# Kernel optimization log

Hardware: AMD Instinct MI355X
Metric: run time of the kernel (lower is better)

## Reference

```python
import jax, jax.numpy as jnp
import numpy as np

B, S, H = 4, 1024, 1024
R = 512          # num_rules
M = 1024         # memory_size
HEADS = 16
STEPS = 3        # inference_steps
TEMP = 1.0       # softmax_temperature
LN_EPS = 1e-5


def setup_inputs() -> dict:
    key = jax.random.key(0)
    ks = jax.random.split(key, 40)
    std = 0.02
    p = lambda k, shp: (jax.random.normal(k, shp, jnp.float32) * std)
    inp = {
        "hidden_states": jax.random.normal(ks[0], (B, S, H), jnp.float32),
        "rule_embeddings": p(ks[1], (R, H)),
        "rule_sel_w": p(ks[2], (H, R)), "rule_sel_b": jnp.zeros((R,), jnp.float32),
        # self-attention (nn.MultiheadAttention) projections
        "attn_wq": p(ks[3], (H, H)), "attn_bq": jnp.zeros((H,), jnp.float32),
        "attn_wk": p(ks[4], (H, H)), "attn_bk": jnp.zeros((H,), jnp.float32),
        "attn_wv": p(ks[5], (H, H)), "attn_bv": jnp.zeros((H,), jnp.float32),
        "attn_wo": p(ks[6], (H, H)), "attn_bo": jnp.zeros((H,), jnp.float32),
        # memory bank + key/query/value projections
        "memory": p(ks[7], (M, H)),
        "mem_q_w": p(ks[8], (H, H)), "mem_q_b": jnp.zeros((H,), jnp.float32),
        "mem_k_w": p(ks[9], (H, H)), "mem_k_b": jnp.zeros((H,), jnp.float32),
        "mem_v_w": p(ks[10], (H, H)), "mem_v_b": jnp.zeros((H,), jnp.float32),
        # memory_attention (nn.MultiheadAttention) projections
        "mattn_wq": p(ks[11], (H, H)), "mattn_bq": jnp.zeros((H,), jnp.float32),
        "mattn_wk": p(ks[12], (H, H)), "mattn_bk": jnp.zeros((H,), jnp.float32),
        "mattn_wv": p(ks[13], (H, H)), "mattn_bv": jnp.zeros((H,), jnp.float32),
        "mattn_wo": p(ks[14], (H, H)), "mattn_bo": jnp.zeros((H,), jnp.float32),
        # rule_application: Linear(2H,H)+LN+GELU+Linear(H,H)
        "ra_w1": p(ks[15], (2 * H, H)), "ra_b1": jnp.zeros((H,), jnp.float32),
        "ra_ln_s": jnp.ones((H,), jnp.float32), "ra_ln_b": jnp.zeros((H,), jnp.float32),
        "ra_w2": p(ks[16], (H, H)), "ra_b2": jnp.zeros((H,), jnp.float32),
        # confidence_scorer
        "conf_w": p(ks[17], (H, 1)), "conf_b": jnp.zeros((1,), jnp.float32),
    }
    return inp


def _mha(q_in, k_in, v_in, wq, bq, wk, bk, wv, bv, wo, bo):
    # standard nn.MultiheadAttention math (batch_first, eval mode -> no dropout)
    b, sq, h = q_in.shape
    d = h // HEADS
    qh = (q_in @ wq + bq).reshape(b, sq, HEADS, d)
    kh = (k_in @ wk + bk).reshape(b, -1, HEADS, d)
    vh = (v_in @ wv + bv).reshape(b, -1, HEADS, d)
    scores = jnp.einsum('bqhd,bkhd->bhqk', qh, kh) / jnp.sqrt(jnp.asarray(d, qh.dtype))
    probs = jax.nn.softmax(scores, axis=-1)
    out = jnp.einsum('bhqk,bkhd->bqhd', probs, vh).reshape(b, sq, h)
    return out @ wo + bo


def _ln(x, s, b):
    mu = x.mean(-1, keepdims=True)
    var = ((x - mu) ** 2).mean(-1, keepdims=True)
    return (x - mu) / jnp.sqrt(var + LN_EPS) * s + b


def reference(hidden_states, rule_embeddings, rule_sel_w, rule_sel_b,
              attn_wq, attn_bq, attn_wk, attn_bk, attn_wv, attn_bv, attn_wo, attn_bo,
              memory, mem_q_w, mem_q_b, mem_k_w, mem_k_b, mem_v_w, mem_v_b,
              mattn_wq, mattn_bq, mattn_wk, mattn_bk, mattn_wv, mattn_bv, mattn_wo, mattn_bo,
              ra_w1, ra_b1, ra_ln_s, ra_ln_b, ra_w2, ra_b2, conf_w, conf_b):
    h = hidden_states
    b = h.shape[0]
    # memory keys/values are input-independent: project once, broadcast over batch
    mk = jnp.broadcast_to((memory @ mem_k_w + mem_k_b)[None], (b, M, H))
    mv = jnp.broadcast_to((memory @ mem_v_w + mem_v_b)[None], (b, M, H))
    for _ in range(STEPS):
        # rule routing: soft selection over the rule-embedding table
        rule_probs = jax.nn.softmax((h @ rule_sel_w + rule_sel_b) / TEMP, axis=-1)  # [B,S,R]
        selected = jnp.einsum('bsr,rh->bsh', rule_probs, rule_embeddings)           # [B,S,H]
        # self-attention reasoning
        h = h + _mha(h, h, h, attn_wq, attn_bq, attn_wk, attn_bk,
                     attn_wv, attn_bv, attn_wo, attn_bo)
        # memory attention
        mq = h @ mem_q_w + mem_q_b
        h = h + _mha(mq, mk, mv, mattn_wq, mattn_bq, mattn_wk, mattn_bk,
                     mattn_wv, mattn_bv, mattn_wo, mattn_bo)
        # rule application MLP on [h ; selected_rules]
        x = jnp.concatenate([h, selected], axis=-1)                                  # [B,S,2H]
        u = jax.nn.gelu(_ln(x @ ra_w1 + ra_b1, ra_ln_s, ra_ln_b), approximate=False)
        h = h + (u @ ra_w2 + ra_b2)
    confidence = jax.nn.sigmoid(h @ conf_w + conf_b)  # [B,S,1]
    return h, confidence
```

## Files before the change

kernel.cpp:

```cpp
#include <hip/hip_runtime.h>
#include <stdint.h>

typedef _Float16 f16;
typedef __attribute__((ext_vector_type(4))) float floatx4;
typedef __attribute__((ext_vector_type(8))) f16   f16x8;
typedef __attribute__((ext_vector_type(4))) f16   f16x4;

#define GLD_LDS16(gp, lp)                                                                      \
  __builtin_amdgcn_global_load_lds((const __attribute__((address_space(1))) void*)(uintptr_t)(gp), \
                                   (__attribute__((address_space(3))) void*)(uintptr_t)(lp), 16, 0, 0)

struct SrlOut {
  int n0;
  const float* bias;
  const float* resid;
  float* Cf; f16* Cb;
  int ldcf, ldcb, transV;
  long long sCb, sCh;
};
struct SrlGemmArgs {
  const f16* A; const f16* B;
  int M, N, K, lda, ldb;
  long long sAb, sAh, sBb, sBh;
  float alpha;
  int nOuts;
  SrlOut out[4];
};

template<int BM, int BN, int MINW>
__global__ __launch_bounds__(256, MINW) void srl_gemm(SrlGemmArgs g) {
  constexpr int BK = 64;
  constexpr int ACH = BM / 32;
  constexpr int BCH = BN / 32;
  constexpr int MI  = (BM == 128 && BN == 128) ? 4 : 2;
  constexpr int NI  = (BN == 128) ? 4 : ((BM == 128) ? 4 : 2);
  __shared__ f16 As[BM * BK];
  __shared__ f16 Bs[BN * BK];
  const int tid  = threadIdx.x;
  const int wid  = tid >> 6;
  const int lane = tid & 63;
  const int z  = blockIdx.z, zh = z & 15, zb = z >> 4;

  const int gx = gridDim.x;
  const int NT = gx * gridDim.y;
  const int L  = blockIdx.y * gx + blockIdx.x;
  const int W  = ((NT & 7) == 0) ? ((L & 7) * (NT >> 3) + (L >> 3)) : L;
  const int tn = (W % gx) * BN;
  const int tm = (W / gx) * BM;

  const f16* Ab = g.A + (long long)zb * g.sAb + (long long)zh * g.sAh + (long long)tm * g.lda;
  const f16* Bb = g.B + (long long)zb * g.sBb + (long long)zh * g.sBh + (long long)tn * g.ldb;
  const int maxAr = g.M - 1 - tm;
  const int maxBr = g.N - 1 - tn;

  int aR[ACH], aO[ACH];
#pragma unroll
  for (int i = 0; i < ACH; ++i) {
    int e = wid * (BM * 16) + i * 512 + lane * 8;
    int r = e >> 6, s = (e >> 3) & 7;
    aR[i] = r; aO[i] = ((s - r) & 7) * 8;
  }
  int bR[BCH], bO[BCH];
#pragma unroll
  for (int i = 0; i < BCH; ++i) {
    int e = wid * (BN * 16) + i * 512 + lane * 8;
    int r = e >> 6, s = (e >> 3) & 7;
    bR[i] = r; bO[i] = ((s - r) & 7) * 8;
  }
  f16* lA = As + wid * (BM * 16);
  f16* lB = Bs + wid * (BN * 16);

  floatx4 acc[MI][NI];
#pragma unroll
  for (int a = 0; a < MI; ++a)
#pragma unroll
    for (int b = 0; b < NI; ++b) {
      acc[a][b][0] = 0.f; acc[a][b][1] = 0.f; acc[a][b][2] = 0.f; acc[a][b][3] = 0.f;
    }

  const int wm = (BM == 128 && BN == 128) ? (wid & 1) * 64
               : (BN == 128)              ? 0
               : (BM == 128)              ? wid * 32
                                          : (wid & 1) * 32;
  const int wn = (BM == 128 && BN == 128) ? (wid >> 1) * 64
               : (BM == 64 && BN == 64)   ? (wid >> 1) * 32
                                          : 0;
  const int lm = lane & 15;
  const int quad = lane >> 4;

  for (int k0 = 0; k0 < g.K; k0 += BK) {
    __syncthreads();
#pragma unroll
    for (int i = 0; i < ACH; ++i) {
      int r = aR[i] <= maxAr ? aR[i] : maxAr;
      GLD_LDS16(Ab + (long long)r * g.lda + (k0 + aO[i]), lA + i * 512);
    }
#pragma unroll
    for (int i = 0; i < BCH; ++i) {
      int r = bR[i] <= maxBr ? bR[i] : maxBr;
      GLD_LDS16(Bb + (long long)r * g.ldb + (k0 + bO[i]), lB + i * 512);
    }
    __syncthreads();
#pragma unroll
    for (int ks = 0; ks < 2; ++ks) {
      f16x8 af[MI], bfr[NI];
#pragma unroll
      for (int mi = 0; mi < MI; ++mi) {
        int row = wm + mi * 16 + lm;
        int sg = ((ks * 4 + quad) + row) & 7;
        af[mi] = *(const f16x8*)(As + row * 64 + sg * 8);
      }
#pragma unroll
      for (int ni = 0; ni < NI; ++ni) {
        int row = wn + ni * 16 + lm;
        int sg = ((ks * 4 + quad) + row) & 7;
        bfr[ni] = *(const f16x8*)(Bs + row * 64 + sg * 8);
      }
#pragma unroll
      for (int mi = 0; mi < MI; ++mi)
#pragma unroll
        for (int ni = 0; ni < NI; ++ni)
          acc[mi][ni] = __builtin_amdgcn_mfma_f32_16x16x32_f16(af[mi], bfr[ni], acc[mi][ni], 0, 0, 0);
    }
  }

  int oi = 0;
  for (int j = 1; j < g.nOuts; ++j)
    if (tn >= g.out[j].n0) oi = j;
  const SrlOut O = g.out[oi];
  const long long zc = (long long)zb * O.sCb + (long long)zh * O.sCh;
#pragma unroll
  for (int mi = 0; mi < MI; ++mi) {
#pragma unroll
    for (int r = 0; r < 4; ++r) {
      int m = tm + wm + mi * 16 + quad * 4 + r;
      if (m >= g.M) continue;
#pragma unroll
      for (int ni = 0; ni < NI; ++ni) {
        int n = tn + wn + ni * 16 + lm;
        if (n >= g.N) continue;
        int nl = n - O.n0;
        float v = acc[mi][ni][r] * g.alpha;
        if (O.bias)  v += O.bias[nl];
        if (O.resid) v += O.resid[(long long)m * O.ldcf + nl];
        if (O.Cf)    O.Cf[zc + (long long)m * O.ldcf + nl] = v;
        if (O.Cb) {
          long long idx = O.transV
              ? ((long long)(m >> 10) * 1048576 + (long long)nl * 1024 + (m & 1023))
              : (zc + (long long)m * O.ldcb + nl);
          O.Cb[idx] = (f16)v;
        }
      }
    }
  }
}

__global__ __launch_bounds__(512, 4) void srl_gemm_p(SrlGemmArgs g) {
  __shared__ f16 As[2][8192];
  __shared__ f16 Bs[2][8192];
  const int tid  = threadIdx.x;
  const int wid  = tid >> 6;
  const int lane = tid & 63;

  const int gx  = gridDim.x;
  const int NTt = gx * gridDim.y;
  const int L   = blockIdx.y * gx + blockIdx.x;
  const int W   = ((NTt & 7) == 0) ? ((L & 7) * (NTt >> 3) + (L >> 3)) : L;
  const int tn  = (W % gx) * 128;
  const int tm  = (W / gx) * 128;

  const f16* Ab = g.A + (long long)tm * g.lda;
  const f16* Bb = g.B + (long long)tn * g.ldb;

  int aR[2], aO[2];
#pragma unroll
  for (int i = 0; i < 2; ++i) {
    int e = wid * 1024 + i * 512 + lane * 8;
    int r = e >> 6, s = (e >> 3) & 7;
    aR[i] = r; aO[i] = ((s - r) & 7) * 8;
  }

  const int wm = (wid >> 1) * 32;
  const int wn = (wid & 1) * 64;
  const int lm = lane & 15;
  const int quad = lane >> 4;

  floatx4 acc[2][4];
#pragma unroll
  for (int a = 0; a < 2; ++a)
#pragma unroll
    for (int b = 0; b < 4; ++b) {
      acc[a][b][0] = 0.f; acc[a][b][1] = 0.f; acc[a][b][2] = 0.f; acc[a][b][3] = 0.f;
    }

  const int nk = g.K >> 6;

  auto stage = [&](int kt, int bsel) {
    const int k0 = kt << 6;
    f16* lA = &As[bsel][0] + wid * 1024;
    f16* lB = &Bs[bsel][0] + wid * 1024;
#pragma unroll
    for (int i = 0; i < 2; ++i)
      GLD_LDS16(Ab + (long long)aR[i] * g.lda + (k0 + aO[i]), lA + i * 512);
#pragma unroll
    for (int i = 0; i < 2; ++i)
      GLD_LDS16(Bb + (long long)aR[i] * g.ldb + (k0 + aO[i]), lB + i * 512);
  };

  stage(0, 0);
  asm volatile("s_waitcnt vmcnt(0)" ::: "memory");
  __builtin_amdgcn_s_barrier();

  auto onestep = [&](int t, int cb) {
    if (t + 1 < nk) stage(t + 1, cb ^ 1);
    asm volatile("" ::: "memory");
    const f16* Asb = &As[cb][0];
    const f16* Bsb = &Bs[cb][0];
#pragma unroll
    for (int ks = 0; ks < 2; ++ks) {
      f16x8 af[2], bfr[4];
#pragma unroll
      for (int mi = 0; mi < 2; ++mi) {
        int row = wm + mi * 16 + lm;
        int sg = ((ks * 4 + quad) + row) & 7;
        af[mi] = *(const f16x8*)(Asb + row * 64 + sg * 8);
      }
#pragma unroll
      for (int ni = 0; ni < 4; ++ni) {
        int row = wn + ni * 16 + lm;
        int sg = ((ks * 4 + quad) + row) & 7;
        bfr[ni] = *(const f16x8*)(Bsb + row * 64 + sg * 8);
      }
#pragma unroll
      for (int mi = 0; mi < 2; ++mi)
#pragma unroll
        for (int ni = 0; ni < 4; ++ni)
          acc[mi][ni] = __builtin_amdgcn_mfma_f32_16x16x32_f16(af[mi], bfr[ni], acc[mi][ni], 0, 0, 0);
    }
    asm volatile("s_waitcnt vmcnt(0) lgkmcnt(0)" ::: "memory");
    __builtin_amdgcn_s_barrier();
  };

  for (int t = 0; t < nk; t += 2) {
    onestep(t, 0);
    onestep(t + 1, 1);
  }

  int oi = 0;
  for (int j = 1; j < g.nOuts; ++j)
    if (tn >= g.out[j].n0) oi = j;
  const SrlOut O = g.out[oi];
#pragma unroll
  for (int mi = 0; mi < 2; ++mi) {
#pragma unroll
    for (int r = 0; r < 4; ++r) {
      int m = tm + wm + mi * 16 + quad * 4 + r;
#pragma unroll
      for (int ni = 0; ni < 4; ++ni) {
        int n = tn + wn + ni * 16 + lm;
        int nl = n - O.n0;
        float v = acc[mi][ni][r] * g.alpha;
        if (O.bias)  v += O.bias[nl];
        if (O.resid) v += O.resid[(long long)m * O.ldcf + nl];
        if (O.Cf)    O.Cf[(long long)m * O.ldcf + nl] = v;
        if (O.Cb) {
          long long idx = O.transV
              ? ((long long)(m >> 10) * 1048576 + (long long)nl * 1024 + (m & 1023))
              : ((long long)m * O.ldcb + nl);
          O.Cb[idx] = (f16)v;
        }
      }
    }
  }
}

struct SrlFlashArgs {
  const f16* Q; const f16* K; const f16* VT; f16* O;
  long long sQb, sKb, sVb;
  float scale;
};

__global__ __launch_bounds__(256, 2) void srl_flash(SrlFlashArgs a) {
  __shared__ f16 Qs[8192];
  __shared__ f16 Ks[8192];
  __shared__ f16 VTs[8192];
  __shared__ f16 Ps[4][4096];
  const int tid = threadIdx.x, wid = tid >> 6, lane = tid & 63;
  const int quad = lane >> 4, c = lane & 15;
  const int L = blockIdx.x;
  const int bh = (L & 7) + ((L >> 6) << 3);
  const int qt = (L >> 3) & 7;
  const int b = bh >> 4, h = bh & 15;
  const f16* Qg = a.Q + (long long)b * a.sQb + (long long)qt * 131072 + h * 64;
  const f16* Kg = a.K + (long long)b * a.sKb + h * 64;
  const f16* Vg = a.VT + (long long)b * a.sVb + (long long)h * 65536;
  f16* Og = a.O + (long long)b * 1048576 + (long long)qt * 131072 + h * 64;

  int rRow[4], rOff[4];
#pragma unroll
  for (int i = 0; i < 4; ++i) {
    int e = wid * 2048 + i * 512 + lane * 8;
    int r = e >> 6, gL = (e >> 3) & 7;
    rRow[i] = r; rOff[i] = ((gL - r) & 7) * 8;
  }
  int vRow[4], vOff[4];
#pragma unroll
  for (int i = 0; i < 4; ++i) {
    int e = wid * 2048 + i * 512 + lane * 8;
    int d = e >> 7, gL = (e >> 3) & 15;
    vRow[i] = d; vOff[i] = ((gL - (d & 7)) & 15) * 8;
  }

#pragma unroll
  for (int i = 0; i < 4; ++i)
    GLD_LDS16(Qg + (long long)rRow[i] * 1024 + rOff[i], Qs + wid * 2048 + i * 512);
  __syncthreads();

  const int wq = wid * 32;
  f16x8 qf[2][2];
#pragma unroll
  for (int nf = 0; nf < 2; ++nf)
#pragma unroll
    for (int ch = 0; ch < 2; ++ch) {
      int row = wq + nf * 16 + c;
      int slot = ((ch * 4 + quad) + row) & 7;
      f16x8 v = *(const f16x8*)(Qs + row * 64 + slot * 8);
      f16 sc = (f16)a.scale;
#pragma unroll
      for (int j = 0; j < 8; ++j) v[j] = v[j] * sc;
      qf[nf][ch] = v;
    }

  float l_s[2] = {0.f, 0.f};
  floatx4 Oa[2][4];
#pragma unroll
  for (int nf = 0; nf < 2; ++nf)
#pragma unroll
    for (int no = 0; no < 4; ++no) {
      Oa[nf][no][0] = 0.f; Oa[nf][no][1] = 0.f; Oa[nf][no][2] = 0.f; Oa[nf][no][3] = 0.f;
    }

  for (int t = 0; t < 8; ++t) {
    __syncthreads();
#pragma unroll
    for (int i = 0; i < 4; ++i)
      GLD_LDS16(Kg + (long long)(t * 128 + rRow[i]) * 1024 + rOff[i], Ks + wid * 2048 + i * 512);
#pragma unroll
    for (int i = 0; i < 4; ++i)
      GLD_LDS16(Vg + (long long)vRow[i] * 1024 + (t * 128 + vOff[i]), VTs + wid * 2048 + i * 512);
    __syncthreads();

    floatx4 sT[2][8];
#pragma unroll
    for (int nf = 0; nf < 2; ++nf)
#pragma unroll
      for (int mf = 0; mf < 8; ++mf) {
        sT[nf][mf][0] = 0.f; sT[nf][mf][1] = 0.f; sT[nf][mf][2] = 0.f; sT[nf][mf][3] = 0.f;
      }
#pragma unroll
    for (int ch = 0; ch < 2; ++ch)
#pragma unroll
      for (int mf = 0; mf < 8; ++mf) {
        int key = mf * 16 + c;
        int slot = ((ch * 4 + quad) + key) & 7;
        f16x8 kf = *(const f16x8*)(Ks + key * 64 + slot * 8);
        sT[0][mf] = __builtin_amdgcn_mfma_f32_16x16x32_f16(kf, qf[0][ch], sT[0][mf], 0, 0, 0);
        sT[1][mf] = __builtin_amdgcn_mfma_f32_16x16x32_f16(kf, qf[1][ch], sT[1][mf], 0, 0, 0);
      }

#pragma unroll
    for (int nf = 0; nf < 2; ++nf) {
      float lt = 0.f;
      const int q = nf * 16 + c;
#pragma unroll
      for (int mf = 0; mf < 8; ++mf) {
        f16x4 pk;
#pragma unroll
        for (int r = 0; r < 4; ++r) {
          float p = __builtin_amdgcn_exp2f(sT[nf][mf][r]);
          lt += p;
          pk[r] = (f16)p;
        }
        int kg = mf * 2 + (quad >> 1), sub = (quad & 1) * 4;
        int slot = (kg + (q & 7)) & 15;
        *(f16x4*)(Ps[wid] + q * 128 + slot * 8 + sub) = pk;
      }
      lt += __shfl_xor(lt, 16);
      lt += __shfl_xor(lt, 32);
      l_s[nf] += lt;
    }
#pragma unroll
    for (int cc = 0; cc < 4; ++cc) {
      f16x8 af[2];
#pragma unroll
      for (int nf = 0; nf < 2; ++nf) {
        int q = nf * 16 + c;
        int slot = ((cc * 4 + quad) + (q & 7)) & 15;
        af[nf] = *(const f16x8*)(Ps[wid] + q * 128 + slot * 8);
      }
#pragma unroll
      for (int no = 0; no < 4; ++no) {
        int d = no * 16 + c;
        int slot = ((cc * 4 + quad) + (d & 7)) & 15;
        f16x8 vf = *(const f16x8*)(VTs + d * 128 + slot * 8);
        Oa[0][no] = __builtin_amdgcn_mfma_f32_16x16x32_f16(af[0], vf, Oa[0][no], 0, 0, 0);
        Oa[1][no] = __builtin_amdgcn_mfma_f32_16x16x32_f16(af[1], vf, Oa[1][no], 0, 0, 0);
      }
    }
  }

#pragma unroll
  for (int nf = 0; nf < 2; ++nf)
#pragma unroll
    for (int r = 0; r < 4; ++r) {
      float li = 1.f / __shfl(l_s[nf], quad * 4 + r);
      int qrow = wq + nf * 16 + quad * 4 + r;
#pragma unroll
      for (int no = 0; no < 4; ++no)
        Qs[qrow * 64 + no * 16 + c] = (f16)(Oa[nf][no][r] * li);
    }
  __syncthreads();
#pragma unroll
  for (int i = 0; i < 4; ++i) {
    int e = wid * 2048 + i * 512 + lane * 8;
    int row = e >> 6, col = e & 63;
    *(f16x8*)(Og + (long long)row * 1024 + col) = *(const f16x8*)(Qs + e);
  }
}

__global__ __launch_bounds__(256) void srl_softmax_rule(const float* logits, f16* probs) {
  __shared__ float red[16];
  const long long row = blockIdx.x;
  const float* p = logits + row * 512;
  const int tid = threadIdx.x;
  float v0 = p[tid], v1 = p[tid + 256];
  float mx = fmaxf(v0, v1);
#pragma unroll
  for (int o = 32; o > 0; o >>= 1) mx = fmaxf(mx, __shfl_down(mx, o));
  const int wid = tid >> 6, lane = tid & 63;
  if (lane == 0) red[wid] = mx;
  __syncthreads();
  if (tid == 0) red[8] = fmaxf(fmaxf(red[0], red[1]), fmaxf(red[2], red[3]));
  __syncthreads();
  mx = red[8];
  float e0 = __expf(v0 - mx), e1 = __expf(v1 - mx);
  float s = e0 + e1;
#pragma unroll
  for (int o = 32; o > 0; o >>= 1) s += __shfl_down(s, o);
  if (lane == 0) red[wid + 4] = s;
  __syncthreads();
  if (tid == 0) red[9] = 1.f / (red[4] + red[5] + red[6] + red[7]);
  __syncthreads();
  const float inv = red[9];
  probs[row * 512 + tid] = (f16)(e0 * inv);
  probs[row * 512 + tid + 256] = (f16)(e1 * inv);
}

__global__ __launch_bounds__(256) void srl_ln_gelu(const float* x, const float* gam, const float* bet, f16* out) {
  __shared__ float red[16];
  const long long row = blockIdx.x;
  const float* p = x + row * 1024;
  const int tid = threadIdx.x;
  float4 xv = *(const float4*)(p + tid * 4);
  float v[4] = {xv.x, xv.y, xv.z, xv.w};
  float s = v[0] + v[1] + v[2] + v[3];
  float s2 = v[0] * v[0] + v[1] * v[1] + v[2] * v[2] + v[3] * v[3];
#pragma unroll
  for (int o = 32; o > 0; o >>= 1) { s += __shfl_down(s, o); s2 += __shfl_down(s2, o); }
  const int wid = tid >> 6, lane = tid & 63;
  if (lane == 0) { red[wid] = s; red[wid + 4] = s2; }
  __syncthreads();
  if (tid == 0) {
    float ts = red[0] + red[1] + red[2] + red[3];
    float ts2 = red[4] + red[5] + red[6] + red[7];
    float mu = ts * (1.f / 1024.f);
    float var = ts2 * (1.f / 1024.f) - mu * mu;
    red[8] = mu;
    red[9] = rsqrtf(var + 1e-5f);
  }
  __syncthreads();
  const float mu = red[8], rstd = red[9];
  f16x4 o4;
#pragma unroll
  for (int i = 0; i < 4; ++i) {
    int c = tid * 4 + i;
    float t = (v[i] - mu) * rstd * gam[c] + bet[c];
    float ge = 0.5f * t * (1.f + erff(t * 0.70710678118654752f));
    o4[i] = (f16)ge;
  }
  *(f16x4*)(out + row * 1024 + tid * 4) = o4;
}

struct SrlTcEnt { const float* src; f16* dst; int rows, cols, trans, tileStart; };
struct SrlTcArgs { SrlTcEnt e[16]; };

__global__ __launch_bounds__(256) void srl_convert_weights(SrlTcArgs a) {
  __shared__ float t[32][33];
  const int bt = blockIdx.x;
  int ei = 0;
#pragma unroll
  for (int j = 1; j < 16; ++j)
    if (bt >= a.e[j].tileStart) ei = j;
  SrlTcEnt E = a.e[ei];
  const int lt = bt - E.tileStart;
  const int tcols = E.cols >> 5;
  const int tr = lt / tcols;
  const int tc = lt - tr * tcols;
  const int r = threadIdx.x >> 5;
  const int c = threadIdx.x & 31;
  if (!E.trans) {
#pragma unroll
    for (int p = 0; p < 4; ++p) {
      long long rr = tr * 32 + r + p * 8;
      long long idx = rr * E.cols + tc * 32 + c;
      E.dst[idx] = (f16)E.src[idx];
    }
  } else {
#pragma unroll
    for (int p = 0; p < 4; ++p)
      t[r + p * 8][c] = E.src[(long long)(tr * 32 + r + p * 8) * E.cols + tc * 32 + c];
    __syncthreads();
#pragma unroll
    for (int p = 0; p < 4; ++p)
      E.dst[(long long)(tc * 32 + r + p * 8) * E.rows + tr * 32 + c] = (f16)t[c][r + p * 8];
  }
}

__global__ __launch_bounds__(256) void srl_prep_bias(const float* rsel_b, const float* bq,
                                                     const float* bk, const float* bv,
                                                     const float* bmq, const float* maq_w,
                                                     const float* bmaq,
                                                     float* bias_qkvr, float* bcomp) {
  int i = blockIdx.x * 256 + threadIdx.x;
  if (i < 3584) {
    float v;
    if (i < 512) v = rsel_b[i];
    else if (i < 1536) v = bq[i - 512];
    else if (i < 2560) v = bk[i - 1536];
    else v = bv[i - 2560];
    bias_qkvr[i] = v;
  } else if (i < 3584 + 1024) {
    int m = i - 3584;
    float s = bmaq[m];
    for (int t = 0; t < 1024; ++t) s += bmq[t] * maq_w[(long long)t * 1024 + m];
    bcomp[m] = s;
  }
}

__global__ __launch_bounds__(256) void srl_h_init(const float* hidden, float* hf, f16* hx) {
  long long base = ((long long)blockIdx.x * 256 + threadIdx.x) * 4;
  float4 v = *(const float4*)(hidden + base);
  *(float4*)(hf + base) = v;
  long long row = base >> 10;
  int col = (int)(base & 1023);
  f16x4 b;
  b[0] = (f16)v.x; b[1] = (f16)v.y; b[2] = (f16)v.z; b[3] = (f16)v.w;
  *(f16x4*)(hx + row * 2048 + col) = b;
}

__global__ __launch_bounds__(256) void srl_finalize(const float* hf, const float* w, const float* b,
                                                    float* out, float* conf) {
  const int bid = blockIdx.x;
  if (bid < 4096) {
    long long base = ((long long)bid * 256 + threadIdx.x) * 4;
    *(float4*)(out + base) = *(const float4*)(hf + base);
  } else {
    const int row = (bid - 4096) * 4 + (threadIdx.x >> 6);
    const int lane = threadIdx.x & 63;
    const float* p = hf + (long long)row * 1024;
    float s = 0.f;
    for (int j = lane; j < 1024; j += 64) s += p[j] * w[j];
#pragma unroll
    for (int o = 32; o > 0; o >>= 1) s += __shfl_down(s, o);
    if (lane == 0) conf[row] = 1.f / (1.f + __expf(-(s + b[0])));
  }
}

extern "C" void kernel_launch(void* const* d_in, const int* in_sizes, int n_in,
                              void* d_out, int out_size, void* d_ws, size_t ws_size,
                              hipStream_t stream) {
  (void)in_sizes; (void)n_in; (void)out_size; (void)ws_size;
  const float* in_hidden   = (const float*)d_in[0];
  const float* in_rule_emb = (const float*)d_in[1];
  const float* in_rsel_w   = (const float*)d_in[2];
  const float* in_rsel_b   = (const float*)d_in[3];
  const float* in_attn_wq  = (const float*)d_in[4];
  const float* in_attn_bq  = (const float*)d_in[5];
  const float* in_attn_wk  = (const float*)d_in[6];
  const float* in_attn_bk  = (const float*)d_in[7];
  const float* in_attn_wv  = (const float*)d_in[8];
  const float* in_attn_bv  = (const float*)d_in[9];
  const float* in_attn_wo  = (const float*)d_in[10];
  const float* in_attn_bo  = (const float*)d_in[11];
  const float* in_memory   = (const float*)d_in[12];
  const float* in_mq_w     = (const float*)d_in[13];
  const float* in_mq_b     = (const float*)d_in[14];
  const float* in_mk_w     = (const float*)d_in[15];
  const float* in_mk_b     = (const float*)d_in[16];
  const float* in_mv_w     = (const float*)d_in[17];
  const float* in_mv_b     = (const float*)d_in[18];
  const float* in_maq_w    = (const float*)d_in[19];
  const float* in_maq_b    = (const float*)d_in[20];
  const float* in_mak_w    = (const float*)d_in[21];
  const float* in_mak_b    = (const float*)d_in[22];
  const float* in_mav_w    = (const float*)d_in[23];
  const float* in_mav_b    = (const float*)d_in[24];
  const float* in_mao_w    = (const float*)d_in[25];
  const float* in_mao_b    = (const float*)d_in[26];
  const float* in_ra_w1    = (const float*)d_in[27];
  const float* in_ra_b1    = (const float*)d_in[28];
  const float* in_ln_s     = (const float*)d_in[29];
  const float* in_ln_b     = (const float*)d_in[30];
  const float* in_ra_w2    = (const float*)d_in[31];
  const float* in_ra_b2    = (const float*)d_in[32];
  const float* in_conf_w   = (const float*)d_in[33];
  const float* in_conf_b   = (const float*)d_in[34];

  char* ws = (char*)d_ws;
  size_t off = 0;
  auto alloc = [&](size_t bytes) -> void* {
    void* p = ws + off;
    off = (off + bytes + 255) & ~(size_t)255;
    return p;
  };
  f16* wt_qkvr    = (f16*)alloc(3584 * 1024 * 2);
  float* bias_qkvr= (float*)alloc(3584 * 4);
  f16* wt_attn_o  = (f16*)alloc(1048576 * 2);
  f16* wt_mq_comp = (f16*)alloc(1048576 * 2);
  float* bcomp    = (float*)alloc(1024 * 4);
  f16* wt_mattn_o = (f16*)alloc(1048576 * 2);
  f16* wt_ra1     = (f16*)alloc(2097152 * 2);
  f16* wt_ra2     = (f16*)alloc(1048576 * 2);
  f16* wt_remb    = (f16*)alloc(524288 * 2);
  f16* wt_mem_kv  = (f16*)alloc(2097152 * 2);
  f16* wt_mattn_k = (f16*)alloc(1048576 * 2);
  f16* wt_mattn_v = (f16*)alloc(1048576 * 2);
  f16* mem_h      = (f16*)alloc(1048576 * 2);
  f16* mk_h       = (f16*)alloc(1048576 * 2);
  f16* mv_h       = (f16*)alloc(1048576 * 2);
  f16* mak_h      = (f16*)alloc(1048576 * 2);
  f16* mavT_h     = (f16*)alloc(1048576 * 2);
  float* h_f      = (float*)alloc(4194304 * 4);
  f16* hx         = (f16*)alloc(8388608 * 2);
  f16* q_h        = (f16*)alloc(4194304 * 2);
  f16* k_h        = (f16*)alloc(4194304 * 2);
  f16* vT_h       = (f16*)alloc(4194304 * 2);
  f16* ctx_h      = (f16*)alloc(4194304 * 2);
  f16* u_h        = (f16*)alloc(4194304 * 2);
  char* arena     = (char*)alloc(16777216);
  float* logits_f = (float*)arena;
  f16* probs_h    = (f16*)(arena + 8388608);
  float* ra1_f    = (float*)arena;
  f16* mqw_nt     = (f16*)arena;
  f16* wmaq_t     = (f16*)(arena + 2097152);

  auto mkOut = [](int n0, const float* bias, const float* resid, float* Cf, int ldcf,
                  f16* Cb, int ldcb, int transV, long long sCb, long long sCh) {
    SrlOut o;
    o.n0 = n0; o.bias = bias; o.resid = resid; o.Cf = Cf; o.Cb = Cb;
    o.ldcf = ldcf; o.ldcb = ldcb; o.transV = transV; o.sCb = sCb; o.sCh = sCh;
    return o;
  };
  auto runP = [&](int M, int N, int K, const f16* A, int lda, const f16* B, int ldb,
                  float alpha, SrlGemmArgs g) {
    g.A = A; g.B = B; g.M = M; g.N = N; g.K = K; g.lda = lda; g.ldb = ldb;
    g.sAb = 0; g.sAh = 0; g.sBb = 0; g.sBh = 0; g.alpha = alpha;
    dim3 grid(N / 128, M / 128, 1);
    hipLaunchKernelGGL(srl_gemm_p, grid, dim3(512), 0, stream, g);
  };
  auto runP1 = [&](int M, int N, int K, const f16* A, int lda, const f16* B, int ldb,
                   float alpha, const float* bias, const float* resid, float* Cf, int ldcf,
                   f16* Cb, int ldcb, int transV) {
    SrlGemmArgs g{};
    g.nOuts = 1;
    g.out[0] = mkOut(0, bias, resid, Cf, ldcf, Cb, ldcb, transV, 0, 0);
    runP(M, N, K, A, lda, B, ldb, alpha, g);
  };
  auto runSm1 = [&](int M, int N, int K, const f16* A, int lda, const f16* B, int ldb,
                    float alpha, const float* bias, const float* resid, float* Cf, int ldcf,
                    f16* Cb, int ldcb, int transV) {
    SrlGemmArgs g{};
    g.nOuts = 1;
    g.out[0] = mkOut(0, bias, resid, Cf, ldcf, Cb, ldcb, transV, 0, 0);
    g.A = A; g.B = B; g.M = M; g.N = N; g.K = K; g.lda = lda; g.ldb = ldb;
    g.sAb = 0; g.sAh = 0; g.sBb = 0; g.sBh = 0; g.alpha = alpha;
    dim3 grid((N + 63) / 64, (M + 63) / 64, 1);
    hipLaunchKernelGGL((srl_gemm<64, 64, 4>), grid, dim3(256), 0, stream, g);
  };
  auto runSm = [&](int M, int N, int K, const f16* A, int lda, const f16* B, int ldb,
                   float alpha, SrlGemmArgs g) {
    g.A = A; g.B = B; g.M = M; g.N = N; g.K = K; g.lda = lda; g.ldb = ldb;
    g.sAb = 0; g.sAh = 0; g.sBb = 0; g.sBh = 0; g.alpha = alpha;
    dim3 grid((N + 63) / 64, (M + 63) / 64, 1);
    hipLaunchKernelGGL((srl_gemm<64, 64, 4>), grid, dim3(256), 0, stream, g);
  };

  SrlTcArgs tc;
  int ts = 0;
  auto setent = [&](int i, const float* s, f16* d, int rows, int cols, int trans) {
    tc.e[i].src = s; tc.e[i].dst = d; tc.e[i].rows = rows; tc.e[i].cols = cols;
    tc.e[i].trans = trans; tc.e[i].tileStart = ts;
    ts += (rows / 32) * (cols / 32);
  };
  setent(0,  in_attn_wq, wt_qkvr + 512 * 1024, 1024, 1024, 1);
  setent(1,  in_attn_wk, wt_qkvr + 1536 * 1024, 1024, 1024, 1);
  setent(2,  in_attn_wv, wt_qkvr + 2560 * 1024, 1024, 1024, 1);
  setent(3,  in_rsel_w,  wt_qkvr, 1024, 512, 1);
  setent(4,  in_attn_wo, wt_attn_o, 1024, 1024, 1);
  setent(5,  in_mq_w,    mqw_nt, 1024, 1024, 0);
  setent(6,  in_maq_w,   wmaq_t, 1024, 1024, 1);
  setent(7,  in_mak_w,   wt_mattn_k, 1024, 1024, 1);
  setent(8,  in_mav_w,   wt_mattn_v, 1024, 1024, 1);
  setent(9,  in_mk_w,    wt_mem_kv, 1024, 1024, 1);
  setent(10, in_mv_w,    wt_mem_kv + 1048576, 1024, 1024, 1);
  setent(11, in_mao_w,   wt_mattn_o, 1024, 1024, 1);
  setent(12, in_ra_w1,   wt_ra1, 2048, 1024, 1);
  setent(13, in_ra_w2,   wt_ra2, 1024, 1024, 1);
  setent(14, in_rule_emb, wt_remb, 512, 1024, 1);
  setent(15, in_memory,  mem_h, 1024, 1024, 0);
  hipLaunchKernelGGL(srl_convert_weights, dim3(ts), dim3(256), 0, stream, tc);
  hipLaunchKernelGGL(srl_prep_bias, dim3(18), dim3(256), 0, stream,
                     in_rsel_b, in_attn_bq, in_attn_bk, in_attn_bv,
                     in_mq_b, in_maq_w, in_maq_b, bias_qkvr, bcomp);
  hipLaunchKernelGGL(srl_h_init, dim3(4096), dim3(256), 0, stream, in_hidden, h_f, hx);

  {
    SrlGemmArgs g{};
    g.nOuts = 2;
    g.out[0] = mkOut(0, in_mk_b, nullptr, nullptr, 0, mk_h, 1024, 0, 0, 0);
    g.out[1] = mkOut(1024, in_mv_b, nullptr, nullptr, 0, mv_h, 1024, 0, 0, 0);
    runSm(1024, 2048, 1024, mem_h, 1024, wt_mem_kv, 1024, 1.f, g);
  }
  runSm1(1024, 1024, 1024, mk_h, 1024, wt_mattn_k, 1024, 1.f, in_mak_b, nullptr, nullptr, 0, mak_h, 1024, 0);
  runSm1(1024, 1024, 1024, mv_h, 1024, wt_mattn_v, 1024, 1.f, in_mav_b, nullptr, nullptr, 0, mavT_h, 0, 1);
  runSm1(1024, 1024, 1024, wmaq_t, 1024, mqw_nt, 1024, 1.f, nullptr, nullptr, nullptr, 0, wt_mq_comp, 1024, 0);

  const float kLog2e = 1.4426950408889634f;
  for (int step = 0; step < 3; ++step) {
    {
      SrlGemmArgs g{};
      g.nOuts = 4;
      g.out[0] = mkOut(0,    bias_qkvr,        nullptr, logits_f, 512, nullptr, 0, 0, 0, 0);
      g.out[1] = mkOut(512,  bias_qkvr + 512,  nullptr, nullptr, 0, q_h, 1024, 0, 0, 0);
      g.out[2] = mkOut(1536, bias_qkvr + 1536, nullptr, nullptr, 0, k_h, 1024, 0, 0, 0);
      g.out[3] = mkOut(2560, bias_qkvr + 2560, nullptr, nullptr, 0, vT_h, 0, 1, 0, 0);
      runP(4096, 3584, 1024, hx, 2048, wt_qkvr, 1024, 1.f, g);
    }
    hipLaunchKernelGGL(srl_softmax_rule, dim3(4096), dim3(256), 0, stream, logits_f, probs_h);
    runP1(4096, 1024, 512, probs_h, 512, wt_remb, 512, 1.f, nullptr, nullptr, nullptr, 0, hx + 1024, 2048, 0);
    {
      SrlFlashArgs fa;
      fa.Q = q_h; fa.K = k_h; fa.VT = vT_h; fa.O = ctx_h;
      fa.sQb = 1048576; fa.sKb = 1048576; fa.sVb = 1048576; fa.scale = 0.125f * kLog2e;
      hipLaunchKernelGGL(srl_flash, dim3(512), dim3(256), 0, stream, fa);
    }
    runP1(4096, 1024, 1024, ctx_h, 1024, wt_attn_o, 1024, 1.f, in_attn_bo, h_f, h_f, 1024, hx, 2048, 0);
    runP1(4096, 1024, 1024, hx, 2048, wt_mq_comp, 1024, 1.f, bcomp, nullptr, nullptr, 0, k_h, 1024, 0);
    {
      SrlFlashArgs fa;
      fa.Q = k_h; fa.K = mak_h; fa.VT = mavT_h; fa.O = ctx_h;
      fa.sQb = 1048576; fa.sKb = 0; fa.sVb = 0; fa.scale = 0.125f * kLog2e;
      hipLaunchKernelGGL(srl_flash, dim3(512), dim3(256), 0, stream, fa);
    }
    runP1(4096, 1024, 1024, ctx_h, 1024, wt_mattn_o, 1024, 1.f, in_mao_b, h_f, h_f, 1024, hx, 2048, 0);
    runP1(4096, 1024, 2048, hx, 2048, wt_ra1, 2048, 1.f, in_ra_b1, nullptr, ra1_f, 1024, nullptr, 0, 0);
    hipLaunchKernelGGL(srl_ln_gelu, dim3(4096), dim3(256), 0, stream, ra1_f, in_ln_s, in_ln_b, u_h);
    runP1(4096, 1024, 1024, u_h, 1024, wt_ra2, 1024, 1.f, in_ra_b2, h_f, h_f, 1024, hx, 2048, 0);
  }

  hipLaunchKernelGGL(srl_finalize, dim3(5120), dim3(256), 0, stream, h_f, in_conf_w, in_conf_b,
                     (float*)d_out, (float*)d_out + 4194304);
}
```

Before: 1.154 ms.

## Triple-buffer GEMM LDS pipeline with single barrier and MFMA priority hints

Moves the main GEMM from double to triple buffering in LDS. Loads run two stages ahead with a partial vmcnt wait, so each k-step needs one barrier instead of a full drain. Fragment loads are hoisted ahead of the MFMA block, and s_setprio is raised around MFMA sections in both the GEMM and the attention kernel. The cost is more LDS per block (96KB), so launch bounds drop to 2 blocks per CU, which may reduce latency hiding.

```diff
diff --git a/kernel.cpp b/kernel.cpp
--- a/kernel.cpp
+++ b/kernel.cpp
@@ -155,9 +155,9 @@
   }
 }
 
-__global__ __launch_bounds__(512, 4) void srl_gemm_p(SrlGemmArgs g) {
-  __shared__ f16 As[2][8192];
-  __shared__ f16 Bs[2][8192];
+__global__ __launch_bounds__(512, 2) void srl_gemm_p(SrlGemmArgs g) {
+  __shared__ f16 As[3][8192];
+  __shared__ f16 Bs[3][8192];
   const int tid  = threadIdx.x;
   const int wid  = tid >> 6;
   const int lane = tid & 63;
@@ -207,44 +207,51 @@
       GLD_LDS16(Bb + (long long)aR[i] * g.ldb + (k0 + aO[i]), lB + i * 512);
   };
 
-  stage(0, 0);
-  asm volatile("s_waitcnt vmcnt(0)" ::: "memory");
-  __builtin_amdgcn_s_barrier();
-
-  auto onestep = [&](int t, int cb) {
-    if (t + 1 < nk) stage(t + 1, cb ^ 1);
-    asm volatile("" ::: "memory");
+  auto compute = [&](int cb) {
     const f16* Asb = &As[cb][0];
     const f16* Bsb = &Bs[cb][0];
+    f16x8 af[2][2], bfr[2][4];
 #pragma unroll
     for (int ks = 0; ks < 2; ++ks) {
-      f16x8 af[2], bfr[4];
 #pragma unroll
       for (int mi = 0; mi < 2; ++mi) {
         int row = wm + mi * 16 + lm;
         int sg = ((ks * 4 + quad) + row) & 7;
-        af[mi] = *(const f16x8*)(Asb + row * 64 + sg * 8);
+        af[ks][mi] = *(const f16x8*)(Asb + row * 64 + sg * 8);
       }
 #pragma unroll
       for (int ni = 0; ni < 4; ++ni) {
         int row = wn + ni * 16 + lm;
         int sg = ((ks * 4 + quad) + row) & 7;
-        bfr[ni] = *(const f16x8*)(Bsb + row * 64 + sg * 8);
-      }
+        bfr[ks][ni] = *(const f16x8*)(Bsb + row * 64 + sg * 8);
+      }
+    }
+    __builtin_amdgcn_s_setprio(1);
+#pragma unroll
+    for (int ks = 0; ks < 2; ++ks)
 #pragma unroll
       for (int mi = 0; mi < 2; ++mi)
 #pragma unroll
         for (int ni = 0; ni < 4; ++ni)
-          acc[mi][ni] = __builtin_amdgcn_mfma_f32_16x16x32_f16(af[mi], bfr[ni], acc[mi][ni], 0, 0, 0);
-    }
-    asm volatile("s_waitcnt vmcnt(0) lgkmcnt(0)" ::: "memory");
+          acc[mi][ni] = __builtin_amdgcn_mfma_f32_16x16x32_f16(af[ks][mi], bfr[ks][ni], acc[mi][ni], 0, 0, 0);
+    __builtin_amdgcn_s_setprio(0);
+  };
+
+  stage(0, 0);
+  if (nk > 1) stage(1, 1);
+
+  int cb = 0, sb = 2;
+  for (int t = 0; t < nk - 1; ++t) {
+    asm volatile("s_waitcnt vmcnt(4)" ::: "memory");
     __builtin_amdgcn_s_barrier();
-  };
-
-  for (int t = 0; t < nk; t += 2) {
-    onestep(t, 0);
-    onestep(t + 1, 1);
-  }
+    if (t + 2 < nk) stage(t + 2, sb);
+    compute(cb);
+    cb = (cb == 2) ? 0 : cb + 1;
+    sb = (sb == 2) ? 0 : sb + 1;
+  }
+  asm volatile("s_waitcnt vmcnt(0)" ::: "memory");
+  __builtin_amdgcn_s_barrier();
+  compute(cb);
 
   int oi = 0;
   for (int j = 1; j < g.nOuts; ++j)
@@ -357,6 +364,7 @@
       for (int mf = 0; mf < 8; ++mf) {
         sT[nf][mf][0] = 0.f; sT[nf][mf][1] = 0.f; sT[nf][mf][2] = 0.f; sT[nf][mf][3] = 0.f;
       }
+    __builtin_amdgcn_s_setprio(1);
 #pragma unroll
     for (int ch = 0; ch < 2; ++ch)
 #pragma unroll
@@ -367,6 +375,7 @@
         sT[0][mf] = __builtin_amdgcn_mfma_f32_16x16x32_f16(kf, qf[0][ch], sT[0][mf], 0, 0, 0);
         sT[1][mf] = __builtin_amdgcn_mfma_f32_16x16x32_f16(kf, qf[1][ch], sT[1][mf], 0, 0, 0);
       }
+    __builtin_amdgcn_s_setprio(0);
 
 #pragma unroll
     for (int nf = 0; nf < 2; ++nf) {
@@ -398,6 +407,7 @@
         int slot = ((cc * 4 + quad) + (q & 7)) & 15;
         af[nf] = *(const f16x8*)(Ps[wid] + q * 128 + slot * 8);
       }
+      __builtin_amdgcn_s_setprio(1);
 #pragma unroll
       for (int no = 0; no < 4; ++no) {
         int d = no * 16 + c;
@@ -406,6 +416,7 @@
         Oa[0][no] = __builtin_amdgcn_mfma_f32_16x16x32_f16(af[0], vf, Oa[0][no], 0, 0, 0);
         Oa[1][no] = __builtin_amdgcn_mfma_f32_16x16x32_f16(af[1], vf, Oa[1][no], 0, 0, 0);
       }
+      __builtin_amdgcn_s_setprio(0);
     }
   }
 
```

Result: no change. 1.154 ms (-0.0%).

## Add 128x64 double-buffered GEMM for N=1024 projections and prioritize MFMA in flash

Applied to the files above, without the earlier changes.

Adds a new GEMM kernel with 128x64 tiles, 256 threads, double-buffered LDS and direct global-to-LDS loads, plus an XCD-style block remap. All N=1024 GEMMs in the step loop now use it instead of the 128x128 512-thread kernel. The goal is to launch more blocks for these shapes (512 vs 256) so the device is better filled, and to overlap loads with MFMA. Separately, the flash kernel raises wave priority around its MFMA sections. Smaller tiles reuse less data per load, and the priority hints may do nothing.

```diff
diff --git a/kernel.cpp b/kernel.cpp
--- a/kernel.cpp
+++ b/kernel.cpp
@@ -274,6 +274,129 @@
   }
 }
 
+__global__ __launch_bounds__(256, 3) void srl_gemm_s(SrlGemmArgs g) {
+  __shared__ f16 As[2][8192];
+  __shared__ f16 Bs[2][4096];
+  const int tid  = threadIdx.x;
+  const int wid  = tid >> 6;
+  const int lane = tid & 63;
+
+  const int gx  = gridDim.x;
+  const int NTt = gx * gridDim.y;
+  const int L   = blockIdx.y * gx + blockIdx.x;
+  const int W   = ((NTt & 7) == 0) ? ((L & 7) * (NTt >> 3) + (L >> 3)) : L;
+  const int tn  = (W % gx) * 64;
+  const int tm  = (W / gx) * 128;
+
+  const f16* Ab = g.A + (long long)tm * g.lda;
+  const f16* Bb = g.B + (long long)tn * g.ldb;
+
+  int aR[4], aO[4];
+#pragma unroll
+  for (int i = 0; i < 4; ++i) {
+    int e = wid * 2048 + i * 512 + lane * 8;
+    int r = e >> 6, s = (e >> 3) & 7;
+    aR[i] = r; aO[i] = ((s - r) & 7) * 8;
+  }
+  int bR[2], bO[2];
+#pragma unroll
+  for (int i = 0; i < 2; ++i) {
+    int e = wid * 1024 + i * 512 + lane * 8;
+    int r = e >> 6, s = (e >> 3) & 7;
+    bR[i] = r; bO[i] = ((s - r) & 7) * 8;
+  }
+
+  const int wm = (wid & 1) * 64;
+  const int wn = (wid >> 1) * 32;
+  const int lm = lane & 15;
+  const int quad = lane >> 4;
+
+  floatx4 acc[4][2];
+#pragma unroll
+  for (int a = 0; a < 4; ++a)
+#pragma unroll
+    for (int b = 0; b < 2; ++b) {
+      acc[a][b][0] = 0.f; acc[a][b][1] = 0.f; acc[a][b][2] = 0.f; acc[a][b][3] = 0.f;
+    }
+
+  const int nk = g.K >> 6;
+
+  auto stage = [&](int kt, int bsel) {
+    const int k0 = kt << 6;
+    f16* lA = &As[bsel][0] + wid * 2048;
+    f16* lB = &Bs[bsel][0] + wid * 1024;
+#pragma unroll
+    for (int i = 0; i < 4; ++i)
+      GLD_LDS16(Ab + (long long)aR[i] * g.lda + (k0 + aO[i]), lA + i * 512);
+#pragma unroll
+    for (int i = 0; i < 2; ++i)
+      GLD_LDS16(Bb + (long long)bR[i] * g.ldb + (k0 + bO[i]), lB + i * 512);
+  };
+
+  stage(0, 0);
+  asm volatile("s_waitcnt vmcnt(0)" ::: "memory");
+  __builtin_amdgcn_s_barrier();
+
+  int cur = 0;
+  for (int t = 0; t < nk; ++t) {
+    if (t + 1 < nk) stage(t + 1, cur ^ 1);
+    asm volatile("" ::: "memory");
+    const f16* Asb = &As[cur][0];
+    const f16* Bsb = &Bs[cur][0];
+#pragma unroll
+    for (int ks = 0; ks < 2; ++ks) {
+      f16x8 af[4], bfr[2];
+#pragma unroll
+      for (int mi = 0; mi < 4; ++mi) {
+        int row = wm + mi * 16 + lm;
+        int sg = ((ks * 4 + quad) + row) & 7;
+        af[mi] = *(const f16x8*)(Asb + row * 64 + sg * 8);
+      }
+#pragma unroll
+      for (int ni = 0; ni < 2; ++ni) {
+        int row = wn + ni * 16 + lm;
+        int sg = ((ks * 4 + quad) + row) & 7;
+        bfr[ni] = *(const f16x8*)(Bsb + row * 64 + sg * 8);
+      }
+#pragma unroll
+      for (int mi = 0; mi < 4; ++mi)
+#pragma unroll
+        for (int ni = 0; ni < 2; ++ni)
+          acc[mi][ni] = __builtin_amdgcn_mfma_f32_16x16x32_f16(af[mi], bfr[ni], acc[mi][ni], 0, 0, 0);
+    }
+    asm volatile("s_waitcnt vmcnt(0) lgkmcnt(0)" ::: "memory");
+    __builtin_amdgcn_s_barrier();
+    cur ^= 1;
+  }
+
+  int oi = 0;
+  for (int j = 1; j < g.nOuts; ++j)
+    if (tn >= g.out[j].n0) oi = j;
+  const SrlOut O = g.out[oi];
+#pragma unroll
+  for (int mi = 0; mi < 4; ++mi) {
+#pragma unroll
+    for (int r = 0; r < 4; ++r) {
+      int m = tm + wm + mi * 16 + quad * 4 + r;
+#pragma unroll
+      for (int ni = 0; ni < 2; ++ni) {
+        int n = tn + wn + ni * 16 + lm;
+        int nl = n - O.n0;
+        float v = acc[mi][ni][r] * g.alpha;
+        if (O.bias)  v += O.bias[nl];
+        if (O.resid) v += O.resid[(long long)m * O.ldcf + nl];
+        if (O.Cf)    O.Cf[(long long)m * O.ldcf + nl] = v;
+        if (O.Cb) {
+          long long idx = O.transV
+              ? ((long long)(m >> 10) * 1048576 + (long long)nl * 1024 + (m & 1023))
+              : ((long long)m * O.ldcb + nl);
+          O.Cb[idx] = (f16)v;
+        }
+      }
+    }
+  }
+}
+
 struct SrlFlashArgs {
   const f16* Q; const f16* K; const f16* VT; f16* O;
   long long sQb, sKb, sVb;
@@ -357,6 +480,7 @@
       for (int mf = 0; mf < 8; ++mf) {
         sT[nf][mf][0] = 0.f; sT[nf][mf][1] = 0.f; sT[nf][mf][2] = 0.f; sT[nf][mf][3] = 0.f;
       }
+    __builtin_amdgcn_s_setprio(1);
 #pragma unroll
     for (int ch = 0; ch < 2; ++ch)
 #pragma unroll
@@ -367,6 +491,7 @@
         sT[0][mf] = __builtin_amdgcn_mfma_f32_16x16x32_f16(kf, qf[0][ch], sT[0][mf], 0, 0, 0);
         sT[1][mf] = __builtin_amdgcn_mfma_f32_16x16x32_f16(kf, qf[1][ch], sT[1][mf], 0, 0, 0);
       }
+    __builtin_amdgcn_s_setprio(0);
 
 #pragma unroll
     for (int nf = 0; nf < 2; ++nf) {
@@ -398,6 +523,7 @@
         int slot = ((cc * 4 + quad) + (q & 7)) & 15;
         af[nf] = *(const f16x8*)(Ps[wid] + q * 128 + slot * 8);
       }
+      __builtin_amdgcn_s_setprio(1);
 #pragma unroll
       for (int no = 0; no < 4; ++no) {
         int d = no * 16 + c;
@@ -406,6 +532,7 @@
         Oa[0][no] = __builtin_amdgcn_mfma_f32_16x16x32_f16(af[0], vf, Oa[0][no], 0, 0, 0);
         Oa[1][no] = __builtin_amdgcn_mfma_f32_16x16x32_f16(af[1], vf, Oa[1][no], 0, 0, 0);
       }
+      __builtin_amdgcn_s_setprio(0);
     }
   }
 
@@ -668,13 +795,16 @@
     dim3 grid(N / 128, M / 128, 1);
     hipLaunchKernelGGL(srl_gemm_p, grid, dim3(512), 0, stream, g);
   };
-  auto runP1 = [&](int M, int N, int K, const f16* A, int lda, const f16* B, int ldb,
-                   float alpha, const float* bias, const float* resid, float* Cf, int ldcf,
-                   f16* Cb, int ldcb, int transV) {
+  auto runS = [&](int M, int N, int K, const f16* A, int lda, const f16* B, int ldb,
+                  float alpha, const float* bias, const float* resid, float* Cf, int ldcf,
+                  f16* Cb, int ldcb, int transV) {
     SrlGemmArgs g{};
     g.nOuts = 1;
     g.out[0] = mkOut(0, bias, resid, Cf, ldcf, Cb, ldcb, transV, 0, 0);
-    runP(M, N, K, A, lda, B, ldb, alpha, g);
+    g.A = A; g.B = B; g.M = M; g.N = N; g.K = K; g.lda = lda; g.ldb = ldb;
+    g.sAb = 0; g.sAh = 0; g.sBb = 0; g.sBh = 0; g.alpha = alpha;
+    dim3 grid(N / 64, M / 128, 1);
+    hipLaunchKernelGGL(srl_gemm_s, grid, dim3(256), 0, stream, g);
   };
   auto runSm1 = [&](int M, int N, int K, const f16* A, int lda, const f16* B, int ldb,
                     float alpha, const float* bias, const float* resid, float* Cf, int ldcf,
@@ -747,25 +877,25 @@
       runP(4096, 3584, 1024, hx, 2048, wt_qkvr, 1024, 1.f, g);
     }
     hipLaunchKernelGGL(srl_softmax_rule, dim3(4096), dim3(256), 0, stream, logits_f, probs_h);
-    runP1(4096, 1024, 512, probs_h, 512, wt_remb, 512, 1.f, nullptr, nullptr, nullptr, 0, hx + 1024, 2048, 0);
+    runS(4096, 1024, 512, probs_h, 512, wt_remb, 512, 1.f, nullptr, nullptr, nullptr, 0, hx + 1024, 2048, 0);
     {
       SrlFlashArgs fa;
       fa.Q = q_h; fa.K = k_h; fa.VT = vT_h; fa.O = ctx_h;
       fa.sQb = 1048576; fa.sKb = 1048576; fa.sVb = 1048576; fa.scale = 0.125f * kLog2e;
       hipLaunchKernelGGL(srl_flash, dim3(512), dim3(256), 0, stream, fa);
     }
-    runP1(4096, 1024, 1024, ctx_h, 1024, wt_attn_o, 1024, 1.f, in_attn_bo, h_f, h_f, 1024, hx, 2048, 0);
-    runP1(4096, 1024, 1024, hx, 2048, wt_mq_comp, 1024, 1.f, bcomp, nullptr, nullptr, 0, k_h, 1024, 0);
+    runS(4096, 1024, 1024, ctx_h, 1024, wt_attn_o, 1024, 1.f, in_attn_bo, h_f, h_f, 1024, hx, 2048, 0);
+    runS(4096, 1024, 1024, hx, 2048, wt_mq_comp, 1024, 1.f, bcomp, nullptr, nullptr, 0, k_h, 1024, 0);
     {
       SrlFlashArgs fa;
       fa.Q = k_h; fa.K = mak_h; fa.VT = mavT_h; fa.O = ctx_h;
       fa.sQb = 1048576; fa.sKb = 0; fa.sVb = 0; fa.scale = 0.125f * kLog2e;
       hipLaunchKernelGGL(srl_flash, dim3(512), dim3(256), 0, stream, fa);
     }
-    runP1(4096, 1024, 1024, ctx_h, 1024, wt_mattn_o, 1024, 1.f, in_mao_b, h_f, h_f, 1024, hx, 2048, 0);
-    runP1(4096, 1024, 2048, hx, 2048, wt_ra1, 2048, 1.f, in_ra_b1, nullptr, ra1_f, 1024, nullptr, 0, 0);
+    runS(4096, 1024, 1024, ctx_h, 1024, wt_mattn_o, 1024, 1.f, in_mao_b, h_f, h_f, 1024, hx, 2048, 0);
+    runS(4096, 1024, 2048, hx, 2048, wt_ra1, 2048, 1.f, in_ra_b1, nullptr, ra1_f, 1024, nullptr, 0, 0);
     hipLaunchKernelGGL(srl_ln_gelu, dim3(4096), dim3(256), 0, stream, ra1_f, in_ln_s, in_ln_b, u_h);
-    runP1(4096, 1024, 1024, u_h, 1024, wt_ra2, 1024, 1.f, in_ra_b2, h_f, h_f, 1024, hx, 2048, 0);
+    runS(4096, 1024, 1024, u_h, 1024, wt_ra2, 1024, 1.f, in_ra_b2, h_f, h_f, 1024, hx, 2048, 0);
   }
 
   hipLaunchKernelGGL(srl_finalize, dim3(5120), dim3(256), 0, stream, h_f, in_conf_w, in_conf_b,
```

Measured after the change: 1.137 ms. No clear change (-1.5%).

## Prefetch flash K/V tiles into registers and route small GEMMs to 64x64 kernel

Applied to the files above, without the earlier changes.

The flash-attention kernel now loads the next K/V tile from global memory into registers while the current tile is computed, then writes it to LDS after compute. This replaces the direct global-to-LDS loads that were bracketed by barriers. MFMA sections are wrapped in s_setprio to favour the matrix work. Separately, the single-output 4096-row GEMMs switch from the 128x128 512-thread kernel to the 64x64 256-thread kernel, which gives more blocks at the cost of less reuse per tile. The register prefetch raises VGPR pressure.

```diff
diff --git a/kernel.cpp b/kernel.cpp
--- a/kernel.cpp
+++ b/kernel.cpp
@@ -314,6 +314,20 @@
 #pragma unroll
   for (int i = 0; i < 4; ++i)
     GLD_LDS16(Qg + (long long)rRow[i] * 1024 + rOff[i], Qs + wid * 2048 + i * 512);
+
+  f16x8 kreg[4], vreg[4];
+#pragma unroll
+  for (int i = 0; i < 4; ++i)
+    kreg[i] = *(const f16x8*)(Kg + (long long)rRow[i] * 1024 + rOff[i]);
+#pragma unroll
+  for (int i = 0; i < 4; ++i)
+    vreg[i] = *(const f16x8*)(Vg + (long long)vRow[i] * 1024 + vOff[i]);
+#pragma unroll
+  for (int i = 0; i < 4; ++i)
+    *(f16x8*)(Ks + wid * 2048 + i * 512 + lane * 8) = kreg[i];
+#pragma unroll
+  for (int i = 0; i < 4; ++i)
+    *(f16x8*)(VTs + wid * 2048 + i * 512 + lane * 8) = vreg[i];
   __syncthreads();
 
   const int wq = wid * 32;
@@ -341,14 +355,14 @@
     }
 
   for (int t = 0; t < 8; ++t) {
-    __syncthreads();
-#pragma unroll
-    for (int i = 0; i < 4; ++i)
-      GLD_LDS16(Kg + (long long)(t * 128 + rRow[i]) * 1024 + rOff[i], Ks + wid * 2048 + i * 512);
-#pragma unroll
-    for (int i = 0; i < 4; ++i)
-      GLD_LDS16(Vg + (long long)vRow[i] * 1024 + (t * 128 + vOff[i]), VTs + wid * 2048 + i * 512);
-    __syncthreads();
+    if (t < 7) {
+#pragma unroll
+      for (int i = 0; i < 4; ++i)
+        kreg[i] = *(const f16x8*)(Kg + (long long)((t + 1) * 128 + rRow[i]) * 1024 + rOff[i]);
+#pragma unroll
+      for (int i = 0; i < 4; ++i)
+        vreg[i] = *(const f16x8*)(Vg + (long long)vRow[i] * 1024 + ((t + 1) * 128 + vOff[i]));
+    }
 
     floatx4 sT[2][8];
 #pragma unroll
@@ -357,6 +371,7 @@
       for (int mf = 0; mf < 8; ++mf) {
         sT[nf][mf][0] = 0.f; sT[nf][mf][1] = 0.f; sT[nf][mf][2] = 0.f; sT[nf][mf][3] = 0.f;
       }
+    __builtin_amdgcn_s_setprio(1);
 #pragma unroll
     for (int ch = 0; ch < 2; ++ch)
 #pragma unroll
@@ -367,6 +382,7 @@
         sT[0][mf] = __builtin_amdgcn_mfma_f32_16x16x32_f16(kf, qf[0][ch], sT[0][mf], 0, 0, 0);
         sT[1][mf] = __builtin_amdgcn_mfma_f32_16x16x32_f16(kf, qf[1][ch], sT[1][mf], 0, 0, 0);
       }
+    __builtin_amdgcn_s_setprio(0);
 
 #pragma unroll
     for (int nf = 0; nf < 2; ++nf) {
@@ -398,6 +414,7 @@
         int slot = ((cc * 4 + quad) + (q & 7)) & 15;
         af[nf] = *(const f16x8*)(Ps[wid] + q * 128 + slot * 8);
       }
+      __builtin_amdgcn_s_setprio(1);
 #pragma unroll
       for (int no = 0; no < 4; ++no) {
         int d = no * 16 + c;
@@ -406,6 +423,18 @@
         Oa[0][no] = __builtin_amdgcn_mfma_f32_16x16x32_f16(af[0], vf, Oa[0][no], 0, 0, 0);
         Oa[1][no] = __builtin_amdgcn_mfma_f32_16x16x32_f16(af[1], vf, Oa[1][no], 0, 0, 0);
       }
+      __builtin_amdgcn_s_setprio(0);
+    }
+
+    if (t < 7) {
+      __syncthreads();
+#pragma unroll
+      for (int i = 0; i < 4; ++i)
+        *(f16x8*)(Ks + wid * 2048 + i * 512 + lane * 8) = kreg[i];
+#pragma unroll
+      for (int i = 0; i < 4; ++i)
+        *(f16x8*)(VTs + wid * 2048 + i * 512 + lane * 8) = vreg[i];
+      __syncthreads();
     }
   }
 
@@ -668,17 +697,9 @@
     dim3 grid(N / 128, M / 128, 1);
     hipLaunchKernelGGL(srl_gemm_p, grid, dim3(512), 0, stream, g);
   };
-  auto runP1 = [&](int M, int N, int K, const f16* A, int lda, const f16* B, int ldb,
-                   float alpha, const float* bias, const float* resid, float* Cf, int ldcf,
-                   f16* Cb, int ldcb, int transV) {
-    SrlGemmArgs g{};
-    g.nOuts = 1;
-    g.out[0] = mkOut(0, bias, resid, Cf, ldcf, Cb, ldcb, transV, 0, 0);
-    runP(M, N, K, A, lda, B, ldb, alpha, g);
-  };
-  auto runSm1 = [&](int M, int N, int K, const f16* A, int lda, const f16* B, int ldb,
-                    float alpha, const float* bias, const float* resid, float* Cf, int ldcf,
-                    f16* Cb, int ldcb, int transV) {
+  auto runS = [&](int M, int N, int K, const f16* A, int lda, const f16* B, int ldb,
+                  float alpha, const float* bias, const float* resid, float* Cf, int ldcf,
+                  f16* Cb, int ldcb, int transV) {
     SrlGemmArgs g{};
     g.nOuts = 1;
     g.out[0] = mkOut(0, bias, resid, Cf, ldcf, Cb, ldcb, transV, 0, 0);
@@ -731,9 +752,9 @@
     g.out[1] = mkOut(1024, in_mv_b, nullptr, nullptr, 0, mv_h, 1024, 0, 0, 0);
     runSm(1024, 2048, 1024, mem_h, 1024, wt_mem_kv, 1024, 1.f, g);
   }
-  runSm1(1024, 1024, 1024, mk_h, 1024, wt_mattn_k, 1024, 1.f, in_mak_b, nullptr, nullptr, 0, mak_h, 1024, 0);
-  runSm1(1024, 1024, 1024, mv_h, 1024, wt_mattn_v, 1024, 1.f, in_mav_b, nullptr, nullptr, 0, mavT_h, 0, 1);
-  runSm1(1024, 1024, 1024, wmaq_t, 1024, mqw_nt, 1024, 1.f, nullptr, nullptr, nullptr, 0, wt_mq_comp, 1024, 0);
+  runS(1024, 1024, 1024, mk_h, 1024, wt_mattn_k, 1024, 1.f, in_mak_b, nullptr, nullptr, 0, mak_h, 1024, 0);
+  runS(1024, 1024, 1024, mv_h, 1024, wt_mattn_v, 1024, 1.f, in_mav_b, nullptr, nullptr, 0, mavT_h, 0, 1);
+  runS(1024, 1024, 1024, wmaq_t, 1024, mqw_nt, 1024, 1.f, nullptr, nullptr, nullptr, 0, wt_mq_comp, 1024, 0);
 
   const float kLog2e = 1.4426950408889634f;
   for (int step = 0; step < 3; ++step) {
@@ -747,25 +768,25 @@
       runP(4096, 3584, 1024, hx, 2048, wt_qkvr, 1024, 1.f, g);
     }
     hipLaunchKernelGGL(srl_softmax_rule, dim3(4096), dim3(256), 0, stream, logits_f, probs_h);
-    runP1(4096, 1024, 512, probs_h, 512, wt_remb, 512, 1.f, nullptr, nullptr, nullptr, 0, hx + 1024, 2048, 0);
+    runS(4096, 1024, 512, probs_h, 512, wt_remb, 512, 1.f, nullptr, nullptr, nullptr, 0, hx + 1024, 2048, 0);
     {
       SrlFlashArgs fa;
       fa.Q = q_h; fa.K = k_h; fa.VT = vT_h; fa.O = ctx_h;
       fa.sQb = 1048576; fa.sKb = 1048576; fa.sVb = 1048576; fa.scale = 0.125f * kLog2e;
       hipLaunchKernelGGL(srl_flash, dim3(512), dim3(256), 0, stream, fa);
     }
-    runP1(4096, 1024, 1024, ctx_h, 1024, wt_attn_o, 1024, 1.f, in_attn_bo, h_f, h_f, 1024, hx, 2048, 0);
-    runP1(4096, 1024, 1024, hx, 2048, wt_mq_comp, 1024, 1.f, bcomp, nullptr, nullptr, 0, k_h, 1024, 0);
+    runS(4096, 1024, 1024, ctx_h, 1024, wt_attn_o, 1024, 1.f, in_attn_bo, h_f, h_f, 1024, hx, 2048, 0);
+    runS(4096, 1024, 1024, hx, 2048, wt_mq_comp, 1024, 1.f, bcomp, nullptr, nullptr, 0, k_h, 1024, 0);
     {
       SrlFlashArgs fa;
       fa.Q = k_h; fa.K = mak_h; fa.VT = mavT_h; fa.O = ctx_h;
       fa.sQb = 1048576; fa.sKb = 0; fa.sVb = 0; fa.scale = 0.125f * kLog2e;
       hipLaunchKernelGGL(srl_flash, dim3(512), dim3(256), 0, stream, fa);
     }
-    runP1(4096, 1024, 1024, ctx_h, 1024, wt_mattn_o, 1024, 1.f, in_mao_b, h_f, h_f, 1024, hx, 2048, 0);
-    runP1(4096, 1024, 2048, hx, 2048, wt_ra1, 2048, 1.f, in_ra_b1, nullptr, ra1_f, 1024, nullptr, 0, 0);
+    runS(4096, 1024, 1024, ctx_h, 1024, wt_mattn_o, 1024, 1.f, in_mao_b, h_f, h_f, 1024, hx, 2048, 0);
+    runS(4096, 1024, 2048, hx, 2048, wt_ra1, 2048, 1.f, in_ra_b1, nullptr, ra1_f, 1024, nullptr, 0, 0);
     hipLaunchKernelGGL(srl_ln_gelu, dim3(4096), dim3(256), 0, stream, ra1_f, in_ln_s, in_ln_b, u_h);
-    runP1(4096, 1024, 1024, u_h, 1024, wt_ra2, 1024, 1.f, in_ra_b2, h_f, h_f, 1024, hx, 2048, 0);
+    runS(4096, 1024, 1024, u_h, 1024, wt_ra2, 1024, 1.f, in_ra_b2, h_f, h_f, 1024, hx, 2048, 0);
   }
 
   hipLaunchKernelGGL(srl_finalize, dim3(5120), dim3(256), 0, stream, h_f, in_conf_w, in_conf_b,
```

After: 1.045 ms. 1.1x faster.
